# Kernel tuning notes

Hardware: AMD Instinct MI355X
Metric: run time of the kernel (lower is better)

Reference implementation:

```python
import jax, jax.numpy as jnp
import numpy as np

CH = 16      # channel_n
HID = 128    # hidden_n


def _max_pool3(a):
    # a: [B,1,H,W]; 3x3 max pool, stride 1, padding 1 (matches F.max_pool2d)
    return jax.lax.reduce_window(
        a, -jnp.inf, jax.lax.max,
        window_dimensions=(1, 1, 3, 3),
        window_strides=(1, 1, 1, 1),
        padding=((0, 0), (0, 0), (1, 1), (1, 1)))


def _living_mask(x):
    return _max_pool3(x[:, 3:4]) > 0.1


def _nca_step(x, perceive_w, w1, b1, w2, key):
    pre_life = _living_mask(x)                                  # [B,1,H,W] bool
    # depthwise sobel conv, identical weight layout/groups as torch Conv2d(groups=CH)
    p = jax.lax.conv_general_dilated(
        x, perceive_w, window_strides=(1, 1),
        padding=((1, 1), (1, 1)),
        dimension_numbers=('NCHW', 'OIHW', 'NCHW'),
        feature_group_count=CH)                                  # [B,2*CH,H,W]
    comb = jnp.transpose(jnp.concatenate([x, p], axis=1), (0, 2, 3, 1))  # [B,H,W,3*CH]
    h = jax.nn.relu(comb @ w1 + b1)                              # [B,H,W,HID]
    delta = jnp.transpose(h @ w2, (0, 3, 1, 2))                  # [B,CH,H,W]
    alpha = x[:, 3:4]
    upd = (jax.random.uniform(key, alpha.shape, dtype=x.dtype) < 0.5) & (alpha > 0.1)
    x = x + delta * upd.astype(x.dtype)
    life = pre_life & _living_mask(x)
    return x * life.astype(x.dtype)


def setup_inputs() -> dict:
    key = jax.random.key(0)
    kx, k1, k2 = jax.random.split(key, 3)
    B, H, W = 2, 128, 128
    x = jax.random.uniform(kx, (B, CH, H, W), dtype=jnp.float32)
    sobel_x = jnp.array([[-1., 0., 1.], [-2., 0., 2.], [-1., 0., 1.]], dtype=jnp.float32)
    sobel_y = jnp.array([[-1., -2., -1.], [0., 0., 0.], [1., 2., 1.]], dtype=jnp.float32)
    wx = jnp.tile(sobel_x[None, None], (CH, 1, 1, 1))
    wy = jnp.tile(sobel_y[None, None], (CH, 1, 1, 1))
    perceive_w = jnp.concatenate([wx, wy], axis=0)               # [2*CH,1,3,3]
    w1 = jax.random.normal(k1, (CH * 3, HID), dtype=jnp.float32) * 0.02
    b1 = jnp.zeros((HID,), dtype=jnp.float32)
    w2 = jax.random.normal(k2, (HID, CH), dtype=jnp.float32) * 0.02
    return {"x": x, "perceive_w": perceive_w, "w1": w1, "b1": b1, "w2": w2, "steps": 64}


def reference(x, perceive_w, w1, b1, w2, steps):
    keys = jax.random.split(jax.random.key(42), steps)

    def body(carry, k):
        return _nca_step(carry, perceive_w, w1, b1, w2, k), None

    x, _ = jax.lax.scan(body, x, keys)
    return x
```

## Files before the change

kernel.cpp:

```cpp
#include <hip/hip_runtime.h>
#include <stdint.h>

#define HH 128
#define WW 128
#define CHN 16
#define NPIX (HH*WW)
#define PLANE (CHN*NPIX)
#define STEPS 64
#define TW 8
#define TH 8

#define AS1 __attribute__((address_space(1)))
#define AS3 __attribute__((address_space(3)))

__device__ __forceinline__ void dma4(const float* g, float* l) {
  __builtin_amdgcn_global_load_lds((const AS1 float*)g, (AS3 float*)l, 4, 0, 0);
}

__host__ __device__ __forceinline__ uint32_t rotl32_(uint32_t x, int d) {
  return (x << d) | (x >> (32 - d));
}

__host__ __device__ __forceinline__ void tf2x32(uint32_t k0, uint32_t k1,
                                                uint32_t x0, uint32_t x1,
                                                uint32_t* o0, uint32_t* o1) {
  uint32_t ks0 = k0, ks1 = k1, ks2 = k0 ^ k1 ^ 0x1BD11BDAu;
  x0 += ks0; x1 += ks1;
  x0 += x1; x1 = rotl32_(x1, 13); x1 ^= x0;
  x0 += x1; x1 = rotl32_(x1, 15); x1 ^= x0;
  x0 += x1; x1 = rotl32_(x1, 26); x1 ^= x0;
  x0 += x1; x1 = rotl32_(x1, 6);  x1 ^= x0;
  x0 += ks1; x1 += ks2 + 1u;
  x0 += x1; x1 = rotl32_(x1, 17); x1 ^= x0;
  x0 += x1; x1 = rotl32_(x1, 29); x1 ^= x0;
  x0 += x1; x1 = rotl32_(x1, 16); x1 ^= x0;
  x0 += x1; x1 = rotl32_(x1, 24); x1 ^= x0;
  x0 += ks2; x1 += ks0 + 2u;
  x0 += x1; x1 = rotl32_(x1, 13); x1 ^= x0;
  x0 += x1; x1 = rotl32_(x1, 15); x1 ^= x0;
  x0 += x1; x1 = rotl32_(x1, 26); x1 ^= x0;
  x0 += x1; x1 = rotl32_(x1, 6);  x1 ^= x0;
  x0 += ks0; x1 += ks1 + 3u;
  x0 += x1; x1 = rotl32_(x1, 17); x1 ^= x0;
  x0 += x1; x1 = rotl32_(x1, 29); x1 ^= x0;
  x0 += x1; x1 = rotl32_(x1, 16); x1 ^= x0;
  x0 += x1; x1 = rotl32_(x1, 24); x1 ^= x0;
  x0 += ks1; x1 += ks2 + 4u;
  x0 += x1; x1 = rotl32_(x1, 13); x1 ^= x0;
  x0 += x1; x1 = rotl32_(x1, 15); x1 ^= x0;
  x0 += x1; x1 = rotl32_(x1, 26); x1 ^= x0;
  x0 += x1; x1 = rotl32_(x1, 6);  x1 ^= x0;
  x0 += ks2; x1 += ks0 + 5u;
  *o0 = x0; *o1 = x1;
}

__global__ void prep_w1t(const float* __restrict__ w1, float* __restrict__ w1t,
                         float* __restrict__ zpad) {
  int i = blockIdx.x * 256 + threadIdx.x;
  if (i < 48 * 128) {
    int j = i / 48, k = i % 48;
    w1t[i] = w1[k * 128 + j];
  }
  if (blockIdx.x == 0 && threadIdx.x < 64) zpad[threadIdx.x] = 0.f;
}

template <int MASKED>
__global__ __launch_bounds__(512, 4) void nca_step(
    const float* __restrict__ xin, const float* __restrict__ plin,
    const float* __restrict__ pw, const float* __restrict__ w1t,
    const float* __restrict__ b1, const float* __restrict__ w2,
    const float* __restrict__ zpad,
    float* __restrict__ xout, float* __restrict__ plout,
    uint32_t k0, uint32_t k1)
{
  __shared__ float xtL[CHN * 100];
  __shared__ float AxtL[144];
  __shared__ float plL[100];
  __shared__ float Lf[100];
  __shared__ float combS[64][49];
  __shared__ uint32_t uBits[64];
  __shared__ float dbuf[8][64][17];

  const int tid = threadIdx.x;
  const int blk = blockIdx.x;
  const int b  = blk >> 8;
  const int oh = ((blk >> 4) & 15) * TH;
  const int ow = (blk & 15) * TW;
  const float* xb = xin + (size_t)b * PLANE;

  if (MASKED) {
    const float* ax = xb + 3 * NPIX;
    if (tid < 144) {
      int r = tid / 12, c = tid % 12;
      int gh = oh + r - 2, gw = ow + c - 2;
      const float* g = (gh >= 0 && gh < HH && gw >= 0 && gw < WW)
                           ? &ax[gh * WW + gw] : zpad;
      dma4(g, &AxtL[tid]);
    }
    const float* pl = plin + b * NPIX;
    if (tid < 100) {
      int r = tid / 10, c = tid % 10;
      int gh = oh + r - 1, gw = ow + c - 1;
      const float* g = (gh >= 0 && gh < HH && gw >= 0 && gw < WW)
                           ? &pl[gh * WW + gw] : zpad;
      dma4(g, &plL[tid]);
    }
  }
  for (int i = tid; i < CHN * 100; i += 512) {
    int c = i / 100, rem = i % 100;
    int r = rem / 10, cc = rem % 10;
    int gh = oh + r - 1, gw = ow + cc - 1;
    const float* g = (gh >= 0 && gh < HH && gw >= 0 && gw < WW)
                         ? &xb[(c * HH + gh) * WW + gw] : zpad;
    dma4(g, &xtL[i]);
  }

  const int wv   = __builtin_amdgcn_readfirstlane((int)threadIdx.x) >> 6;
  const int lane = tid & 63;

  if (wv == 0) {
    const int gr = (oh + (lane >> 3)) * WW + ow + (lane & 7);
    uint32_t o0, o1;
    tf2x32(k0, k1, 0u, (uint32_t)(b * NPIX + gr), &o0, &o1);
    uBits[lane] = o0 ^ o1;
  }
  __syncthreads();

  if (MASKED) {
    if (tid < 100) {
      int r = tid / 10, c = tid % 10;
      float m = AxtL[r * 12 + c];
      m = fmaxf(m, AxtL[r * 12 + c + 1]);        m = fmaxf(m, AxtL[r * 12 + c + 2]);
      m = fmaxf(m, AxtL[(r + 1) * 12 + c]);      m = fmaxf(m, AxtL[(r + 1) * 12 + c + 1]);
      m = fmaxf(m, AxtL[(r + 1) * 12 + c + 2]);  m = fmaxf(m, AxtL[(r + 2) * 12 + c]);
      m = fmaxf(m, AxtL[(r + 2) * 12 + c + 1]);  m = fmaxf(m, AxtL[(r + 2) * 12 + c + 2]);
      Lf[tid] = (m > 0.1f && plL[tid] > 0.5f) ? 1.f : 0.f;
    }
    __syncthreads();
  }

  {
    const int pr = lane >> 3, pc = lane & 7;
    const int cA = 2 * wv, cB = 2 * wv + 1;
    float nA[9], nB[9];
    #pragma unroll
    for (int dy = 0; dy < 3; ++dy)
      #pragma unroll
      for (int dx = 0; dx < 3; ++dx) {
        const int idx = (pr + dy) * 10 + (pc + dx);
        const float lfv = MASKED ? Lf[idx] : 1.f;
        nA[dy * 3 + dx] = xtL[cA * 100 + idx] * lfv;
        nB[dy * 3 + dx] = xtL[cB * 100 + idx] * lfv;
      }
    float pA0 = 0.f, pA1 = 0.f, pB0 = 0.f, pB1 = 0.f;
    #pragma unroll
    for (int i = 0; i < 9; ++i) {
      pA0 = fmaf(pw[(2 * cA) * 9 + i],     nA[i], pA0);
      pA1 = fmaf(pw[(2 * cA + 1) * 9 + i], nA[i], pA1);
      pB0 = fmaf(pw[(2 * cB) * 9 + i],     nB[i], pB0);
      pB1 = fmaf(pw[(2 * cB + 1) * 9 + i], nB[i], pB1);
    }
    combS[lane][cA] = nA[4];
    combS[lane][cB] = nB[4];
    combS[lane][16 + 2 * cA] = pA0;
    combS[lane][17 + 2 * cA] = pA1;
    combS[lane][16 + 2 * cB] = pB0;
    combS[lane][17 + 2 * cB] = pB1;
    if (wv == 1) {
      float m = nB[0];
      #pragma unroll
      for (int i = 1; i < 9; ++i) m = fmaxf(m, nB[i]);
      plout[b * NPIX + (oh + pr) * WW + (ow + pc)] = (m > 0.1f) ? 1.f : 0.f;
    }
  }
  __syncthreads();

  const int jbase = wv * 16;
  float comb[48];
  {
    const float* cr = &combS[lane][0];
    #pragma unroll
    for (int q = 0; q < 12; ++q) {
      float4 v = *(const float4*)(cr + 4 * q);
      comb[4 * q] = v.x; comb[4 * q + 1] = v.y;
      comb[4 * q + 2] = v.z; comb[4 * q + 3] = v.w;
    }
  }
  #pragma unroll
  for (int k = 0; k < 48; ++k) asm volatile("" : "+v"(comb[k]));

  float delta[16];
  #pragma unroll
  for (int c = 0; c < 16; ++c) delta[c] = 0.f;
  for (int jj = 0; jj < 16; jj += 2) {
    const int j0 = jbase + jj;
    const float* wr0 = w1t + j0 * 48;
    const float* wr1 = wr0 + 48;
    float h0 = b1[j0], h1 = b1[j0 + 1];
    #pragma unroll
    for (int k = 0; k < 48; ++k) {
      h0 = fmaf(comb[k], wr0[k], h0);
      h1 = fmaf(comb[k], wr1[k], h1);
    }
    h0 = fmaxf(h0, 0.f); h1 = fmaxf(h1, 0.f);
    const float* w20 = w2 + j0 * 16;
    #pragma unroll
    for (int c = 0; c < 16; ++c)
      delta[c] = fmaf(h0, w20[c], fmaf(h1, w20[16 + c], delta[c]));
  }

  #pragma unroll
  for (int c = 0; c < 16; ++c) dbuf[wv][lane][c] = delta[c];
  __syncthreads();

  const float u = (((uBits[lane] >> 31) == 0u) && (comb[3] > 0.1f)) ? 1.f : 0.f;
  const int gidx = (oh + (lane >> 3)) * WW + (ow + (lane & 7));
  float* qb = xout + (size_t)b * PLANE;
  #pragma unroll
  for (int c2 = 0; c2 < 2; ++c2) {
    const int c = 2 * wv + c2;
    float s = dbuf[0][lane][c];
    #pragma unroll
    for (int t = 1; t < 8; ++t) s += dbuf[t][lane][c];
    qb[c * NPIX + gidx] = fmaf(s, u, comb[c]);
  }
}

__global__ __launch_bounds__(256, 2) void nca_fin(
    const float* __restrict__ xl, const float* __restrict__ pl,
    float* __restrict__ out)
{
  __shared__ float Axt[TH + 4][TW + 4];
  const int tid = threadIdx.x;
  const int blk = blockIdx.x;
  const int b  = blk >> 8;
  const int oh = ((blk >> 4) & 15) * TH;
  const int ow = (blk & 15) * TW;
  const float* ax = xl + (size_t)b * PLANE + 3 * NPIX;
  for (int i = tid; i < (TH + 4) * (TW + 4); i += 256) {
    int r = i / (TW + 4), c = i % (TW + 4);
    int gh = oh + r - 2, gw = ow + c - 2;
    Axt[r][c] = (gh >= 0 && gh < HH && gw >= 0 && gw < WW)
                    ? ax[gh * WW + gw] : 0.f;
  }
  __syncthreads();
  const int wv = tid >> 6, lane = tid & 63;
  const int pr = lane >> 3, pc = lane & 7;
  const int gidx = (oh + pr) * WW + (ow + pc);
  float m = Axt[pr + 1][pc + 1];
  #pragma unroll
  for (int dy = 0; dy < 3; ++dy)
    #pragma unroll
    for (int dx = 0; dx < 3; ++dx)
      m = fmaxf(m, Axt[pr + 1 + dy][pc + 1 + dx]);
  const float lf = (m > 0.1f && pl[b * NPIX + gidx] > 0.5f) ? 1.f : 0.f;
  const float* qb = xl + (size_t)b * PLANE;
  float* ob = out + (size_t)b * PLANE;
  #pragma unroll
  for (int c2 = 0; c2 < 4; ++c2) {
    const int c = wv * 4 + c2;
    ob[c * NPIX + gidx] = qb[c * NPIX + gidx] * lf;
  }
}

extern "C" void kernel_launch(void* const* d_in, const int* in_sizes, int n_in,
                              void* d_out, int out_size, void* d_ws, size_t ws_size,
                              hipStream_t stream) {
  (void)in_sizes; (void)n_in; (void)out_size; (void)ws_size;
  const float* x  = (const float*)d_in[0];
  const float* pw = (const float*)d_in[1];
  const float* w1 = (const float*)d_in[2];
  const float* b1 = (const float*)d_in[3];
  const float* w2 = (const float*)d_in[4];

  float* out = (float*)d_out;
  float* ws  = (float*)d_ws;
  float* xb0 = ws;
  float* xb1 = ws + 2 * PLANE;
  float* pb0 = ws + 4 * PLANE;
  float* pb1 = ws + 4 * PLANE + 2 * NPIX;
  float* w1t = ws + 4 * PLANE + 4 * NPIX;
  float* zpad = w1t + 48 * 128;

  prep_w1t<<<(48 * 128 + 255) / 256, 256, 0, stream>>>(w1, w1t, zpad);

  uint32_t key0[STEPS], key1[STEPS];
  for (uint32_t s = 0; s < STEPS; ++s)
    tf2x32(0u, 42u, 0u, s, &key0[s], &key1[s]);

  float* xbuf[2] = { xb0, xb1 };
  float* pbuf[2] = { pb0, pb1 };
  nca_step<0><<<dim3(512), dim3(512), 0, stream>>>(
      x, nullptr, pw, w1t, b1, w2, zpad, xbuf[0], pbuf[0], key0[0], key1[0]);
  for (int s = 1; s < STEPS; ++s) {
    nca_step<1><<<dim3(512), dim3(512), 0, stream>>>(
        xbuf[(s - 1) & 1], pbuf[(s - 1) & 1], pw, w1t, b1, w2, zpad,
        xbuf[s & 1], pbuf[s & 1], key0[s], key1[s]);
  }
  const int lf = (STEPS - 1) & 1;
  nca_fin<<<dim3(512), dim3(256), 0, stream>>>(xbuf[lf], pbuf[lf], out);
}
```

Baseline: 1.300 ms.

## Replace LDS DMA loads with plain loads and defer RNG to epilogue

Halo tiles are now loaded with ordinary global loads and LDS stores instead of global_load_lds DMA through a zero-pad buffer. The previous-life value is read directly from global memory inside the mask computation rather than staged in LDS. The Threefry RNG moves from the prologue to the epilogue, where it is combined with the alpha test into a float mask in LDS. This removes the zpad buffer and the uBits barrier, and takes the RNG work off the critical path before the conv. The trade-off is losing asynchronous DMA and paying register-staged loads instead.

```diff
diff --git a/kernel.cpp b/kernel.cpp
--- a/kernel.cpp
+++ b/kernel.cpp
@@ -9,13 +9,6 @@
 #define STEPS 64
 #define TW 8
 #define TH 8
-
-#define AS1 __attribute__((address_space(1)))
-#define AS3 __attribute__((address_space(3)))
-
-__device__ __forceinline__ void dma4(const float* g, float* l) {
-  __builtin_amdgcn_global_load_lds((const AS1 float*)g, (AS3 float*)l, 4, 0, 0);
-}
 
 __host__ __device__ __forceinline__ uint32_t rotl32_(uint32_t x, int d) {
   return (x << d) | (x >> (32 - d));
@@ -54,14 +47,12 @@
   *o0 = x0; *o1 = x1;
 }
 
-__global__ void prep_w1t(const float* __restrict__ w1, float* __restrict__ w1t,
-                         float* __restrict__ zpad) {
+__global__ void prep_w1t(const float* __restrict__ w1, float* __restrict__ w1t) {
   int i = blockIdx.x * 256 + threadIdx.x;
   if (i < 48 * 128) {
     int j = i / 48, k = i % 48;
     w1t[i] = w1[k * 128 + j];
   }
-  if (blockIdx.x == 0 && threadIdx.x < 64) zpad[threadIdx.x] = 0.f;
 }
 
 template <int MASKED>
@@ -69,16 +60,14 @@
     const float* __restrict__ xin, const float* __restrict__ plin,
     const float* __restrict__ pw, const float* __restrict__ w1t,
     const float* __restrict__ b1, const float* __restrict__ w2,
-    const float* __restrict__ zpad,
     float* __restrict__ xout, float* __restrict__ plout,
     uint32_t k0, uint32_t k1)
 {
   __shared__ float xtL[CHN * 100];
   __shared__ float AxtL[144];
-  __shared__ float plL[100];
   __shared__ float Lf[100];
   __shared__ float combS[64][49];
-  __shared__ uint32_t uBits[64];
+  __shared__ float uLDS[64];
   __shared__ float dbuf[8][64][17];
 
   const int tid = threadIdx.x;
@@ -93,51 +82,40 @@
     if (tid < 144) {
       int r = tid / 12, c = tid % 12;
       int gh = oh + r - 2, gw = ow + c - 2;
-      const float* g = (gh >= 0 && gh < HH && gw >= 0 && gw < WW)
-                           ? &ax[gh * WW + gw] : zpad;
-      dma4(g, &AxtL[tid]);
-    }
+      AxtL[tid] = (gh >= 0 && gh < HH && gw >= 0 && gw < WW)
+                      ? ax[gh * WW + gw] : 0.f;
+    }
+  }
+  for (int i = tid; i < CHN * 100; i += 512) {
+    int c = i / 100, rem = i % 100;
+    int r = rem / 10, cc = rem % 10;
+    int gh = oh + r - 1, gw = ow + cc - 1;
+    xtL[i] = (gh >= 0 && gh < HH && gw >= 0 && gw < WW)
+                 ? xb[(c * HH + gh) * WW + gw] : 0.f;
+  }
+  __syncthreads();
+
+  if (MASKED) {
     const float* pl = plin + b * NPIX;
     if (tid < 100) {
       int r = tid / 10, c = tid % 10;
       int gh = oh + r - 1, gw = ow + c - 1;
-      const float* g = (gh >= 0 && gh < HH && gw >= 0 && gw < WW)
-                           ? &pl[gh * WW + gw] : zpad;
-      dma4(g, &plL[tid]);
-    }
-  }
-  for (int i = tid; i < CHN * 100; i += 512) {
-    int c = i / 100, rem = i % 100;
-    int r = rem / 10, cc = rem % 10;
-    int gh = oh + r - 1, gw = ow + cc - 1;
-    const float* g = (gh >= 0 && gh < HH && gw >= 0 && gw < WW)
-                         ? &xb[(c * HH + gh) * WW + gw] : zpad;
-    dma4(g, &xtL[i]);
+      float life = 0.f;
+      if (gh >= 0 && gh < HH && gw >= 0 && gw < WW) {
+        float m = AxtL[r * 12 + c];
+        m = fmaxf(m, AxtL[r * 12 + c + 1]);        m = fmaxf(m, AxtL[r * 12 + c + 2]);
+        m = fmaxf(m, AxtL[(r + 1) * 12 + c]);      m = fmaxf(m, AxtL[(r + 1) * 12 + c + 1]);
+        m = fmaxf(m, AxtL[(r + 1) * 12 + c + 2]);  m = fmaxf(m, AxtL[(r + 2) * 12 + c]);
+        m = fmaxf(m, AxtL[(r + 2) * 12 + c + 1]);  m = fmaxf(m, AxtL[(r + 2) * 12 + c + 2]);
+        if (m > 0.1f && pl[gh * WW + gw] > 0.5f) life = 1.f;
+      }
+      Lf[tid] = life;
+    }
+    __syncthreads();
   }
 
   const int wv   = __builtin_amdgcn_readfirstlane((int)threadIdx.x) >> 6;
   const int lane = tid & 63;
-
-  if (wv == 0) {
-    const int gr = (oh + (lane >> 3)) * WW + ow + (lane & 7);
-    uint32_t o0, o1;
-    tf2x32(k0, k1, 0u, (uint32_t)(b * NPIX + gr), &o0, &o1);
-    uBits[lane] = o0 ^ o1;
-  }
-  __syncthreads();
-
-  if (MASKED) {
-    if (tid < 100) {
-      int r = tid / 10, c = tid % 10;
-      float m = AxtL[r * 12 + c];
-      m = fmaxf(m, AxtL[r * 12 + c + 1]);        m = fmaxf(m, AxtL[r * 12 + c + 2]);
-      m = fmaxf(m, AxtL[(r + 1) * 12 + c]);      m = fmaxf(m, AxtL[(r + 1) * 12 + c + 1]);
-      m = fmaxf(m, AxtL[(r + 1) * 12 + c + 2]);  m = fmaxf(m, AxtL[(r + 2) * 12 + c]);
-      m = fmaxf(m, AxtL[(r + 2) * 12 + c + 1]);  m = fmaxf(m, AxtL[(r + 2) * 12 + c + 2]);
-      Lf[tid] = (m > 0.1f && plL[tid] > 0.5f) ? 1.f : 0.f;
-    }
-    __syncthreads();
-  }
 
   {
     const int pr = lane >> 3, pc = lane & 7;
@@ -211,9 +189,16 @@
 
   #pragma unroll
   for (int c = 0; c < 16; ++c) dbuf[wv][lane][c] = delta[c];
-  __syncthreads();
-
-  const float u = (((uBits[lane] >> 31) == 0u) && (comb[3] > 0.1f)) ? 1.f : 0.f;
+  if (wv == 0) {
+    const int gr = (oh + (lane >> 3)) * WW + ow + (lane & 7);
+    uint32_t o0, o1;
+    tf2x32(k0, k1, 0u, (uint32_t)(b * NPIX + gr), &o0, &o1);
+    const uint32_t bits = o0 ^ o1;
+    uLDS[lane] = (((bits >> 31) == 0u) && (combS[lane][3] > 0.1f)) ? 1.f : 0.f;
+  }
+  __syncthreads();
+
+  const float u = uLDS[lane];
   const int gidx = (oh + (lane >> 3)) * WW + (ow + (lane & 7));
   float* qb = xout + (size_t)b * PLANE;
   #pragma unroll
@@ -280,9 +265,8 @@
   float* pb0 = ws + 4 * PLANE;
   float* pb1 = ws + 4 * PLANE + 2 * NPIX;
   float* w1t = ws + 4 * PLANE + 4 * NPIX;
-  float* zpad = w1t + 48 * 128;
-
-  prep_w1t<<<(48 * 128 + 255) / 256, 256, 0, stream>>>(w1, w1t, zpad);
+
+  prep_w1t<<<(48 * 128 + 255) / 256, 256, 0, stream>>>(w1, w1t);
 
   uint32_t key0[STEPS], key1[STEPS];
   for (uint32_t s = 0; s < STEPS; ++s)
@@ -291,10 +275,10 @@
   float* xbuf[2] = { xb0, xb1 };
   float* pbuf[2] = { pb0, pb1 };
   nca_step<0><<<dim3(512), dim3(512), 0, stream>>>(
-      x, nullptr, pw, w1t, b1, w2, zpad, xbuf[0], pbuf[0], key0[0], key1[0]);
+      x, nullptr, pw, w1t, b1, w2, xbuf[0], pbuf[0], key0[0], key1[0]);
   for (int s = 1; s < STEPS; ++s) {
     nca_step<1><<<dim3(512), dim3(512), 0, stream>>>(
-        xbuf[(s - 1) & 1], pbuf[(s - 1) & 1], pw, w1t, b1, w2, zpad,
+        xbuf[(s - 1) & 1], pbuf[(s - 1) & 1], pw, w1t, b1, w2,
         xbuf[s & 1], pbuf[s & 1], key0[s], key1[s]);
   }
   const int lf = (STEPS - 1) & 1;
```

New measurement: 1.319 ms. Within noise of the previous version (+1.5%).
